# Performance work log

Measured on AMD Instinct MI355X. Metric: run time of the kernel, lower is better.

Reference implementation:

```python
import jax, jax.numpy as jnp
import numpy as np

SL, BS, E, H, PF, STRIDE, SHIFT = 2048, 2, 1024, 16, 16, 1, 0
DH = E // H  # 64


def setup_inputs() -> dict:
    key = jax.random.key(0)
    ks = jax.random.split(key, 6)
    s = 0.02
    return {
        'x': jax.random.normal(ks[0], (SL, BS, E), jnp.float32),
        'ln_g': jnp.ones((E,), jnp.float32),
        'ln_b': jnp.zeros((E,), jnp.float32),
        'Wq': jax.random.normal(ks[1], (E, E), jnp.float32) * s,
        'bq': jnp.zeros((E,), jnp.float32),
        'Wk': jax.random.normal(ks[2], (E, E), jnp.float32) * s,
        'bk': jnp.zeros((E,), jnp.float32),
        'Wv': jax.random.normal(ks[3], (E, E), jnp.float32) * s,
        'bv': jnp.zeros((E,), jnp.float32),
        'Wo': jax.random.normal(ks[4], (E, E), jnp.float32) * s,
        'bo': jnp.zeros((E,), jnp.float32),
    }


def _layernorm(x, g, b, eps=1e-5):
    m = x.mean(-1, keepdims=True)
    v = jnp.var(x, axis=-1, keepdims=True)
    return (x - m) * jax.lax.rsqrt(v + eps) * g + b


def _sparsify(context, h):
    # faithful to sparsify(): r = (arange(h)+1)*stride - pf + shift (+ arange(pf)), mod c
    c = context.shape[0]
    base = (jnp.arange(h) + 1) * STRIDE - PF + SHIFT          # [h]
    idx = (base[None, :] + jnp.arange(PF)[:, None]) % c       # [pf, h]
    return context[idx.reshape(-1)].reshape(PF, h, context.shape[1], context.shape[2])


def reference(x, ln_g, ln_b, Wq, bq, Wk, bk, Wv, bv, Wo, bo):
    sl, bs, e = x.shape
    residual = x
    xn = _layernorm(x, ln_g, ln_b)
    # gather pf-sized local context window per query position (modular wrap)
    fetch = _sparsify(xn, sl)                                  # [pf, sl, bs, E]
    # per-token query (length-1) attending to its pf gathered keys
    q = (xn @ Wq + bq).reshape(sl, bs, H, DH)                  # [sl,bs,H,dh]
    k = (fetch @ Wk + bk).reshape(PF, sl, bs, H, DH)           # [pf,sl,bs,H,dh]
    v = (fetch @ Wv + bv).reshape(PF, sl, bs, H, DH)
    scale = 1.0 / jnp.sqrt(jnp.float32(DH))
    scores = jnp.einsum('sbhd,psbhd->sbhp', q, k) * scale      # [sl,bs,H,pf]
    attn = jax.nn.softmax(scores, axis=-1)
    out = jnp.einsum('sbhp,psbhd->sbhd', attn, v).reshape(sl, bs, e)
    out = out @ Wo + bo                                        # output projection
    # dropout is a no-op in eval
    return residual + out
```

## Files before the change

### kernel.cpp

```cpp
#include <hip/hip_runtime.h>
#include <cstdint>
#include <cstddef>

#define SLEN 2048
#define BSZ  2
#define EDIM 1024
#define NHEAD 16
#define DHEAD 64
#define PFW  16
#define NTOK (SLEN*BSZ)

typedef __attribute__((ext_vector_type(8))) short short8;
typedef __attribute__((ext_vector_type(4))) float floatx4;
typedef __attribute__((ext_vector_type(4))) int   int4v;

__device__ __forceinline__ short f2bf(float f) {
  union { float f; uint32_t u; } v; v.f = f;
  uint32_t r = v.u + 0x7fffu + ((v.u >> 16) & 1u);
  return (short)(r >> 16);
}
__device__ __forceinline__ float bf2f(short s) {
  union { uint32_t u; float f; } v; v.u = ((uint32_t)(uint16_t)s) << 16;
  return v.f;
}
__device__ __forceinline__ int q8(float f, float inv) {
  int q = __float2int_rn(f * inv);
  return min(127, max(-127, q));
}

__device__ __forceinline__ void async16(const void* g, void* l) {
  __builtin_amdgcn_global_load_lds((const __attribute__((address_space(1))) void*)g,
                                   (__attribute__((address_space(3))) void*)l,
                                   16, 0, 0);
}

#define VMCNT(n) asm volatile("s_waitcnt vmcnt(" #n ")" ::: "memory")

__global__ __launch_bounds__(256) void prep_kernel(
    const float* __restrict__ x, const float* __restrict__ g,
    const float* __restrict__ b, char* __restrict__ xn_i8,
    float* __restrict__ xn_scl,
    const float* __restrict__ W0, const float* __restrict__ W1,
    const float* __restrict__ W2, const float* __restrict__ W3,
    short* __restrict__ Wt_base)
{
  const int bid = blockIdx.x;
  const int tid = threadIdx.x;

  if (bid < NTOK) {
    const int row = bid;
    const float4 v = ((const float4*)(x + (size_t)row * EDIM))[tid];
    float s  = v.x + v.y + v.z + v.w;
    float ss = v.x * v.x + v.y * v.y + v.z * v.z + v.w * v.w;
#pragma unroll
    for (int off = 32; off; off >>= 1) {
      s  += __shfl_xor(s, off);
      ss += __shfl_xor(ss, off);
    }
    __shared__ float ws_s[4], ws_ss[4], ws_m[4];
    const int lane = tid & 63, wave = tid >> 6;
    if (lane == 0) { ws_s[wave] = s; ws_ss[wave] = ss; }
    __syncthreads();
    s  = ws_s[0] + ws_s[1] + ws_s[2] + ws_s[3];
    ss = ws_ss[0] + ws_ss[1] + ws_ss[2] + ws_ss[3];

    const float mean = s * (1.0f / EDIM);
    const float var  = ss * (1.0f / EDIM) - mean * mean;
    const float rs   = rsqrtf(var + 1e-5f);

    const float4 gv = ((const float4*)g)[tid];
    const float4 bv = ((const float4*)b)[tid];
    const float n0 = (v.x - mean) * rs * gv.x + bv.x;
    const float n1 = (v.y - mean) * rs * gv.y + bv.y;
    const float n2 = (v.z - mean) * rs * gv.z + bv.z;
    const float n3 = (v.w - mean) * rs * gv.w + bv.w;

    float am = fmaxf(fmaxf(fabsf(n0), fabsf(n1)), fmaxf(fabsf(n2), fabsf(n3)));
#pragma unroll
    for (int off = 32; off; off >>= 1) am = fmaxf(am, __shfl_xor(am, off));
    if (lane == 0) ws_m[wave] = am;
    __syncthreads();
    am = fmaxf(fmaxf(ws_m[0], ws_m[1]), fmaxf(ws_m[2], ws_m[3]));

    const float inv = (am > 1e-30f) ? 127.0f / am : 0.0f;
    const int q0 = q8(n0, inv), q1 = q8(n1, inv), q2 = q8(n2, inv), q3 = q8(n3, inv);
    const uint32_t pack = (uint32_t)(q0 & 0xff) | ((uint32_t)(q1 & 0xff) << 8) |
                          ((uint32_t)(q2 & 0xff) << 16) | ((uint32_t)(q3 & 0xff) << 24);
    ((uint32_t*)(xn_i8 + (size_t)row * EDIM))[tid] = pack;
    if (tid == 0) xn_scl[row] = am * (1.0f / 127.0f);
  } else {
    const int t = bid - NTOK;
    const int z = t >> 10;
    const int rem = t & 1023;
    const int n0 = (rem & 31) * 32;
    const int k0 = (rem >> 5) * 32;
    const float* W = (z == 0) ? W0 : (z == 1) ? W1 : (z == 2) ? W2 : W3;
    short* Wt = Wt_base + (size_t)z * EDIM * EDIM;

    __shared__ float tile[32][33];
    const int tx = tid & 31;
    const int ty = tid >> 5;
#pragma unroll
    for (int i = 0; i < 4; ++i)
      tile[ty + i * 8][tx] = W[(size_t)(k0 + ty + i * 8) * EDIM + n0 + tx];
    __syncthreads();
#pragma unroll
    for (int i = 0; i < 4; ++i)
      Wt[(size_t)(n0 + ty + i * 8) * EDIM + k0 + tx] = f2bf(tile[tx][ty + i * 8]);
  }
}

__global__ __launch_bounds__(256) void quant_w(
    const short* __restrict__ Wt, char* __restrict__ w_i8,
    float* __restrict__ w_scl)
{
  const int R = blockIdx.x;
  const int tid = threadIdx.x;
  const short4 s4 = ((const short4*)(Wt + (size_t)R * EDIM))[tid];
  const float w0 = bf2f(s4.x), w1 = bf2f(s4.y), w2 = bf2f(s4.z), w3 = bf2f(s4.w);

  float am = fmaxf(fmaxf(fabsf(w0), fabsf(w1)), fmaxf(fabsf(w2), fabsf(w3)));
#pragma unroll
  for (int off = 32; off; off >>= 1) am = fmaxf(am, __shfl_xor(am, off));
  __shared__ float wm[4];
  const int lane = tid & 63, wave = tid >> 6;
  if (lane == 0) wm[wave] = am;
  __syncthreads();
  am = fmaxf(fmaxf(wm[0], wm[1]), fmaxf(wm[2], wm[3]));

  const float inv = (am > 1e-30f) ? 127.0f / am : 0.0f;
  const int q0 = q8(w0, inv), q1 = q8(w1, inv), q2 = q8(w2, inv), q3 = q8(w3, inv);
  const uint32_t pack = (uint32_t)(q0 & 0xff) | ((uint32_t)(q1 & 0xff) << 8) |
                        ((uint32_t)(q2 & 0xff) << 16) | ((uint32_t)(q3 & 0xff) << 24);
  ((uint32_t*)(w_i8 + (size_t)R * EDIM))[tid] = pack;
  if (tid == 0) w_scl[R] = am * (1.0f / 127.0f);
}

__global__ __launch_bounds__(512, 2) void gemm_qkv256(
    const char* __restrict__ xn_i8, const float* __restrict__ xn_scl,
    const char* __restrict__ w_i8, const float* __restrict__ w_scl,
    const float* __restrict__ bq, const float* __restrict__ bk,
    const float* __restrict__ bv, short* __restrict__ qkv_base)
{
  __shared__ __align__(16) char lds[4][32768];

  const int bid = blockIdx.x;
  const int lin = (bid & 7) * 24 + (bid >> 3);
  const int mt  = lin & 15;
  const int nt  = lin >> 4;
  const int z   = nt >> 2;
  const int bm  = mt * 256;
  const int bnz = (nt & 3) * 256;

  const float* bias = (z == 0) ? bq : (z == 1) ? bk : bv;
  short* out = qkv_base + (size_t)z * NTOK * EDIM;

  const int tid = threadIdx.x;
  const int wv  = tid >> 6;
  const int ln  = tid & 63;
  const int q   = ln >> 4;
  const int l16 = ln & 15;
  const int wm  = wv >> 2;
  const int wn  = wv & 3;

  const int sr = tid >> 2;
  const int sc = ((tid & 3) * 16) ^ ((sr & 3) * 16);
  const char* gA0 = xn_i8 + (size_t)(bm + sr) * EDIM + sc;
  const char* gA1 = gA0 + (size_t)128 * EDIM;
  const char* gB0 = w_i8 + ((size_t)z << 20) + (size_t)(bnz + sr) * EDIM + sc;
  const char* gB1 = gB0 + (size_t)128 * EDIM;
  const int wbase = wv * 1024;

#define QSTAGE(tt) do { \
    char* s_ = lds[(tt) & 3]; \
    async16(gA0 + (tt) * 64, s_ + wbase); \
    async16(gA1 + (tt) * 64, s_ + 8192 + wbase); \
    async16(gB0 + (tt) * 64, s_ + 16384 + wbase); \
    async16(gB1 + (tt) * 64, s_ + 24576 + wbase); \
  } while (0)

  const int swz  = (q * 16) ^ ((l16 & 3) * 16);
  const int aoff = (wm * 128 + l16) * 64 + swz;
  const int boff = 16384 + (wn * 64 + l16) * 64 + swz;

  int4v acc[8][4];
#pragma unroll
  for (int mi = 0; mi < 8; ++mi)
#pragma unroll
    for (int ni = 0; ni < 4; ++ni) { int4v zz = {0, 0, 0, 0}; acc[mi][ni] = zz; }

  QSTAGE(0); QSTAGE(1); QSTAGE(2);
  VMCNT(8);
  __builtin_amdgcn_s_barrier();
  __builtin_amdgcn_sched_barrier(0);

#pragma unroll
  for (int t = 0; t < 16; ++t) {
    if (t + 3 < 16) QSTAGE(t + 3);

    const char* sl = lds[t & 3];
    int4v bf[4], af[8];
#pragma unroll
    for (int ni = 0; ni < 4; ++ni)
      bf[ni] = *(const int4v*)(sl + boff + ni * 1024);
#pragma unroll
    for (int mi = 0; mi < 8; ++mi)
      af[mi] = *(const int4v*)(sl + aoff + mi * 1024);

    __builtin_amdgcn_s_setprio(1);
#pragma unroll
    for (int mi = 0; mi < 8; ++mi)
#pragma unroll
      for (int ni = 0; ni < 4; ++ni)
        acc[mi][ni] = __builtin_amdgcn_mfma_i32_16x16x64_i8(
            af[mi], bf[ni], acc[mi][ni], 0, 0, 0);
    __builtin_amdgcn_s_setprio(0);

    if (t < 15) {
      if (t <= 12)      VMCNT(8);
      else if (t == 13) VMCNT(4);
      else              VMCNT(0);
      __builtin_amdgcn_s_barrier();
      __builtin_amdgcn_sched_barrier(0);
    }
  }
#undef QSTAGE

  const int rbase = bm + wm * 128 + q * 4;
  const int cbl   = bnz + wn * 64 + l16;
#pragma unroll
  for (int mi = 0; mi < 8; ++mi) {
    float sa[4];
#pragma unroll
    for (int r = 0; r < 4; ++r) sa[r] = xn_scl[rbase + mi * 16 + r];
#pragma unroll
    for (int ni = 0; ni < 4; ++ni) {
      const int c  = cbl + ni * 16;
      const float sb = w_scl[z * EDIM + c];
      const float bb = bias[c];
      const int4v v = acc[mi][ni];
#pragma unroll
      for (int r = 0; r < 4; ++r)
        out[(size_t)(rbase + mi * 16 + r) * EDIM + c] =
            f2bf((float)v[r] * (sa[r] * sb) + bb);
    }
  }
}

__global__ __launch_bounds__(256) void gemm_o_bf16(
    const short* __restrict__ Abf, const short* __restrict__ Bt,
    const float* __restrict__ bo, const float* __restrict__ residual,
    float* __restrict__ out)
{
  __shared__ __align__(16) char ring[4][12288];

  const int bm = blockIdx.x * 64;
  const int bn = blockIdx.y * 128;
  const int tid  = threadIdx.x;
  const int lane = tid & 63;
  const int wave = tid >> 6;

  const int lrow = lane >> 2;
  const int scol = ((lane & 3) * 16) ^ ((lrow & 3) * 16);
  const char* gA0 = (const char*)Abf + (size_t)(bm + wave * 16 + lrow) * (EDIM * 2) + scol;
  const char* gB0 = (const char*)Bt  + (size_t)(bn + wave * 32 + lrow) * (EDIM * 2) + scol;
  const char* gB1 = gB0 + (size_t)16 * (EDIM * 2);
  const int aw = wave * 1024;
  const int bw = 4096 + wave * 2048;

#define OSTAGE(tt) do { \
    char* s_ = ring[(tt) & 3]; \
    async16(gA0 + (tt) * 64, s_ + aw); \
    async16(gB0 + (tt) * 64, s_ + bw); \
    async16(gB1 + (tt) * 64, s_ + bw + 1024); \
  } while (0)

  const int wm  = (wave >> 1) * 32;
  const int wn  = (wave & 1) * 64;
  const int l16 = lane & 15;
  const int q4  = lane >> 4;
  const int swz  = (q4 * 16) ^ ((l16 & 3) * 16);
  const int aoff = (wm + l16) * 64 + swz;
  const int boff = 4096 + (wn + l16) * 64 + swz;

  floatx4 facc[2][4];
#pragma unroll
  for (int i = 0; i < 2; ++i)
#pragma unroll
    for (int j = 0; j < 4; ++j) { floatx4 zz = {0.f, 0.f, 0.f, 0.f}; facc[i][j] = zz; }

  OSTAGE(0); OSTAGE(1); OSTAGE(2);
  VMCNT(6);
  __builtin_amdgcn_s_barrier();
  __builtin_amdgcn_sched_barrier(0);

#pragma unroll
  for (int t = 0; t < 32; ++t) {
    if (t + 3 < 32) OSTAGE(t + 3);

    const char* sl = ring[t & 3];
    short8 af[2], bf[4];
#pragma unroll
    for (int mi = 0; mi < 2; ++mi)
      af[mi] = *(const short8*)(sl + aoff + mi * 1024);
#pragma unroll
    for (int ni = 0; ni < 4; ++ni)
      bf[ni] = *(const short8*)(sl + boff + ni * 1024);

    __builtin_amdgcn_s_setprio(1);
#pragma unroll
    for (int mi = 0; mi < 2; ++mi)
#pragma unroll
      for (int ni = 0; ni < 4; ++ni)
        facc[mi][ni] = __builtin_amdgcn_mfma_f32_16x16x32_bf16(
            af[mi], bf[ni], facc[mi][ni], 0, 0, 0);
    __builtin_amdgcn_s_setprio(0);

    if (t < 31) {
      if (t <= 28)      VMCNT(6);
      else if (t == 29) VMCNT(3);
      else              VMCNT(0);
      __builtin_amdgcn_s_barrier();
      __builtin_amdgcn_sched_barrier(0);
    }
  }
#undef OSTAGE

  const int r0 = bm + wm + q4 * 4;
  const int c0 = bn + wn + l16;
#pragma unroll
  for (int mi = 0; mi < 2; ++mi)
#pragma unroll
    for (int ni = 0; ni < 4; ++ni) {
      const int col = c0 + ni * 16;
      const float bb = bo[col];
#pragma unroll
      for (int r = 0; r < 4; ++r) {
        const int row = r0 + mi * 16 + r;
        const size_t idx = (size_t)row * EDIM + col;
        out[idx] = residual[idx] + facc[mi][ni][r] + bb;
      }
    }
}

#define VT_LD 80
#define PB_LD 40

__global__ __launch_bounds__(256) void attn_mfma(
    const short* __restrict__ Q, const short* __restrict__ K,
    const short* __restrict__ V, short* __restrict__ Obf)
{
  const int tid  = threadIdx.x;
  const int lane = tid & 63;
  const int wave = tid >> 6;
  const int quad = lane >> 4;
  const int l16  = lane & 15;

  const int bh = blockIdx.y;
  const int h  = bh & (NHEAD - 1);
  const int b  = bh >> 4;
  const int s_blk = blockIdx.x * 64;
  const int col0  = h * DHEAD;

  __shared__ __align__(16) short VT[64 * VT_LD];
  __shared__ __align__(16) short Pb[4][16 * PB_LD];

  for (int task = tid; task < 320; task += 256) {
    const int kp  = task >> 3;
    const int dg  = task & 7;
    const int kk0 = kp * 2;
    int sA = s_blk - 15 + kk0;
    int sB = sA + 1;
    if (sA < 0) sA += SLEN;  if (sA >= SLEN) sA -= SLEN;
    if (sB < 0) sB += SLEN;  if (sB >= SLEN) sB -= SLEN;
    const short8 vA = *(const short8*)(V + (size_t)(sA * BSZ + b) * EDIM + col0 + dg * 8);
    const short8 vB = *(const short8*)(V + (size_t)(sB * BSZ + b) * EDIM + col0 + dg * 8);
#pragma unroll
    for (int j = 0; j < 8; ++j) {
      const int d = dg * 8 + j;
      const uint32_t pack = (uint32_t)(uint16_t)vA[j] | ((uint32_t)(uint16_t)vB[j] << 16);
      *(uint32_t*)&VT[d * VT_LD + kk0] = pack;
    }
  }

  const int sw = s_blk + wave * 16;
  short8 aq[2];
  {
    const size_t base = (size_t)((sw + l16) * BSZ + b) * EDIM + col0 + quad * 8;
    aq[0] = *(const short8*)(Q + base);
    aq[1] = *(const short8*)(Q + base + 32);
  }
  short8 bkf[2][2];
#pragma unroll
  for (int T = 0; T < 2; ++T) {
    int ks = sw - 15 + T * 16 + l16;
    if (ks < 0) ks += SLEN;
    if (ks >= SLEN) ks -= SLEN;
    const size_t base = (size_t)(ks * BSZ + b) * EDIM + col0 + quad * 8;
    bkf[T][0] = *(const short8*)(K + base);
    bkf[T][1] = *(const short8*)(K + base + 32);
  }

  floatx4 S[2];
  { floatx4 zz = {0.f, 0.f, 0.f, 0.f}; S[0] = zz; S[1] = zz; }
#pragma unroll
  for (int T = 0; T < 2; ++T) {
    S[T] = __builtin_amdgcn_mfma_f32_16x16x32_bf16(aq[0], bkf[T][0], S[T], 0, 0, 0);
    S[T] = __builtin_amdgcn_mfma_f32_16x16x32_bf16(aq[1], bkf[T][1], S[T], 0, 0, 0);
  }

  float sc[2][4];
#pragma unroll
  for (int T = 0; T < 2; ++T)
#pragma unroll
    for (int r = 0; r < 4; ++r) {
      const int m = quad * 4 + r;
      const int c = T * 16 + l16;
      const int d = c - m;
      sc[T][r] = (d >= 0 && d <= 15) ? S[T][r] * 0.125f : -1e30f;
    }
  float mx[4], sm[4];
#pragma unroll
  for (int r = 0; r < 4; ++r) mx[r] = fmaxf(sc[0][r], sc[1][r]);
#pragma unroll
  for (int off = 1; off <= 8; off <<= 1)
#pragma unroll
    for (int r = 0; r < 4; ++r) mx[r] = fmaxf(mx[r], __shfl_xor(mx[r], off));
  float p[2][4];
#pragma unroll
  for (int r = 0; r < 4; ++r) {
    p[0][r] = __expf(sc[0][r] - mx[r]);
    p[1][r] = __expf(sc[1][r] - mx[r]);
    sm[r] = p[0][r] + p[1][r];
  }
#pragma unroll
  for (int off = 1; off <= 8; off <<= 1)
#pragma unroll
    for (int r = 0; r < 4; ++r) sm[r] += __shfl_xor(sm[r], off);

  __syncthreads();

  short* Pw = Pb[wave];
#pragma unroll
  for (int T = 0; T < 2; ++T)
#pragma unroll
    for (int r = 0; r < 4; ++r) {
      const int m = quad * 4 + r;
      const int c = T * 16 + l16;
      Pw[m * PB_LD + c] = f2bf(p[T][r]);
    }
  __syncthreads();
  const short8 ap = *(const short8*)(Pw + l16 * PB_LD + quad * 8);

  floatx4 Oacc[4];
  { floatx4 zz = {0.f, 0.f, 0.f, 0.f}; Oacc[0] = zz; Oacc[1] = zz; Oacc[2] = zz; Oacc[3] = zz; }
#pragma unroll
  for (int nt = 0; nt < 4; ++nt) {
    const short8 bv = *(const short8*)(VT + (nt * 16 + l16) * VT_LD + wave * 16 + quad * 8);
    Oacc[nt] = __builtin_amdgcn_mfma_f32_16x16x32_bf16(ap, bv, Oacc[nt], 0, 0, 0);
  }

  float ism[4];
#pragma unroll
  for (int r = 0; r < 4; ++r) ism[r] = 1.0f / sm[r];
#pragma unroll
  for (int nt = 0; nt < 4; ++nt)
#pragma unroll
    for (int r = 0; r < 4; ++r) {
      const int m = quad * 4 + r;
      const int row = (sw + m) * BSZ + b;
      Obf[(size_t)row * EDIM + col0 + nt * 16 + l16] = f2bf(Oacc[nt][r] * ism[r]);
    }
}

extern "C" void kernel_launch(void* const* d_in, const int* in_sizes, int n_in,
                              void* d_out, int out_size, void* d_ws, size_t ws_size,
                              hipStream_t stream) {
  const float* x    = (const float*)d_in[0];
  const float* ln_g = (const float*)d_in[1];
  const float* ln_b = (const float*)d_in[2];
  const float* Wq   = (const float*)d_in[3];
  const float* bq   = (const float*)d_in[4];
  const float* Wk   = (const float*)d_in[5];
  const float* bk   = (const float*)d_in[6];
  const float* Wv   = (const float*)d_in[7];
  const float* bv   = (const float*)d_in[8];
  const float* Wo   = (const float*)d_in[9];
  const float* bo   = (const float*)d_in[10];
  float* out = (float*)d_out;

  char* ws = (char*)d_ws;
  char*  xn_i8   = ws;
  short* Wt      = (short*)(ws + ((size_t)4  << 20));
  char*  w_i8    = ws + ((size_t)12 << 20);
  short* QKV     = (short*)(ws + ((size_t)16 << 20));
  float* xn_scl  = (float*)(ws + ((size_t)44 << 20));
  float* w_scl   = (float*)(ws + ((size_t)44 << 20) + (1 << 16));
  short* Obf     = (short*)ws;

  prep_kernel<<<NTOK + 4096, 256, 0, stream>>>(x, ln_g, ln_b, xn_i8, xn_scl,
                                               Wq, Wk, Wv, Wo, Wt);
  quant_w<<<3 * EDIM, 256, 0, stream>>>(Wt, w_i8, w_scl);
  gemm_qkv256<<<192, 512, 0, stream>>>(xn_i8, xn_scl, w_i8, w_scl,
                                       bq, bk, bv, QKV);
  attn_mfma<<<dim3(SLEN / 64, BSZ * NHEAD), 256, 0, stream>>>(
      QKV, QKV + (size_t)NTOK * EDIM, QKV + (size_t)2 * NTOK * EDIM, Obf);
  gemm_o_bf16<<<dim3(NTOK / 64, EDIM / 128), 256, 0, stream>>>(
      Obf, Wt + (size_t)3 * EDIM * EDIM, bo, x, out);
}
```

Before: 149.2 us.

## Fuse all stages into a persistent megakernel with grid-wide barriers

Replaces the five separate kernel launches (layernorm/quantize, weight transpose, weight quantize, QKV GEMM, attention, output GEMM) with one persistent 256-block kernel. The stages are separated by a software grid barrier built on atomic flags in the workspace, which is reset with a memset before each launch. The goal is to remove launch overhead and inter-kernel gaps. In exchange, stages now run with a fixed grid of 256 blocks at 512 threads, which may under-occupy some phases. It also relies on all blocks being co-resident, or the barrier can deadlock.

```diff
diff --git a/kernel.cpp b/kernel.cpp
--- a/kernel.cpp
+++ b/kernel.cpp
@@ -7,7 +7,6 @@
 #define EDIM 1024
 #define NHEAD 16
 #define DHEAD 64
-#define PFW  16
 #define NTOK (SLEN*BSZ)
 
 typedef __attribute__((ext_vector_type(8))) short short8;
@@ -27,450 +26,502 @@
   int q = __float2int_rn(f * inv);
   return min(127, max(-127, q));
 }
-
 __device__ __forceinline__ void async16(const void* g, void* l) {
   __builtin_amdgcn_global_load_lds((const __attribute__((address_space(1))) void*)g,
                                    (__attribute__((address_space(3))) void*)l,
                                    16, 0, 0);
 }
-
 #define VMCNT(n) asm volatile("s_waitcnt vmcnt(" #n ")" ::: "memory")
 
-__global__ __launch_bounds__(256) void prep_kernel(
-    const float* __restrict__ x, const float* __restrict__ g,
-    const float* __restrict__ b, char* __restrict__ xn_i8,
-    float* __restrict__ xn_scl,
-    const float* __restrict__ W0, const float* __restrict__ W1,
-    const float* __restrict__ W2, const float* __restrict__ W3,
-    short* __restrict__ Wt_base)
+__device__ __forceinline__ void grid_bar(uint32_t* flags, uint32_t* go,
+                                         int phase, int bid, int tid) {
+  __syncthreads();
+  if (bid == 0) {
+    if (tid > 0 && tid < 256) {
+      while (__hip_atomic_load(&flags[tid], __ATOMIC_ACQUIRE,
+                               __HIP_MEMORY_SCOPE_AGENT) < (uint32_t)phase)
+        __builtin_amdgcn_s_sleep(1);
+    }
+    __syncthreads();
+    if (tid == 0)
+      __hip_atomic_store(go, (uint32_t)phase, __ATOMIC_RELEASE,
+                         __HIP_MEMORY_SCOPE_AGENT);
+  } else {
+    if (tid == 0) {
+      __hip_atomic_store(&flags[bid], (uint32_t)phase, __ATOMIC_RELEASE,
+                         __HIP_MEMORY_SCOPE_AGENT);
+      while (__hip_atomic_load(go, __ATOMIC_ACQUIRE,
+                               __HIP_MEMORY_SCOPE_AGENT) < (uint32_t)phase)
+        __builtin_amdgcn_s_sleep(1);
+    }
+  }
+  __syncthreads();
+}
+
+#define VT_LD 80
+#define PB_LD 40
+
+__global__ __launch_bounds__(512, 2) void mega(
+    const float* __restrict__ x, const float* __restrict__ ln_g,
+    const float* __restrict__ ln_b,
+    const float* __restrict__ Wq, const float* __restrict__ bq,
+    const float* __restrict__ Wk, const float* __restrict__ bk,
+    const float* __restrict__ Wv, const float* __restrict__ bv,
+    const float* __restrict__ Wo, const float* __restrict__ bo,
+    char* xn_i8, float* xn_scl, short* Wt_base, char* w_i8, float* w_scl,
+    short* qkv_base, short* Obf, float* __restrict__ out,
+    uint32_t* bar)
 {
-  const int bid = blockIdx.x;
-  const int tid = threadIdx.x;
-
-  if (bid < NTOK) {
-    const int row = bid;
-    const float4 v = ((const float4*)(x + (size_t)row * EDIM))[tid];
-    float s  = v.x + v.y + v.z + v.w;
-    float ss = v.x * v.x + v.y * v.y + v.z * v.z + v.w * v.w;
-#pragma unroll
-    for (int off = 32; off; off >>= 1) {
-      s  += __shfl_xor(s, off);
-      ss += __shfl_xor(ss, off);
-    }
-    __shared__ float ws_s[4], ws_ss[4], ws_m[4];
-    const int lane = tid & 63, wave = tid >> 6;
-    if (lane == 0) { ws_s[wave] = s; ws_ss[wave] = ss; }
-    __syncthreads();
-    s  = ws_s[0] + ws_s[1] + ws_s[2] + ws_s[3];
-    ss = ws_ss[0] + ws_ss[1] + ws_ss[2] + ws_ss[3];
-
-    const float mean = s * (1.0f / EDIM);
-    const float var  = ss * (1.0f / EDIM) - mean * mean;
-    const float rs   = rsqrtf(var + 1e-5f);
-
-    const float4 gv = ((const float4*)g)[tid];
-    const float4 bv = ((const float4*)b)[tid];
-    const float n0 = (v.x - mean) * rs * gv.x + bv.x;
-    const float n1 = (v.y - mean) * rs * gv.y + bv.y;
-    const float n2 = (v.z - mean) * rs * gv.z + bv.z;
-    const float n3 = (v.w - mean) * rs * gv.w + bv.w;
-
-    float am = fmaxf(fmaxf(fabsf(n0), fabsf(n1)), fmaxf(fabsf(n2), fabsf(n3)));
-#pragma unroll
-    for (int off = 32; off; off >>= 1) am = fmaxf(am, __shfl_xor(am, off));
-    if (lane == 0) ws_m[wave] = am;
-    __syncthreads();
-    am = fmaxf(fmaxf(ws_m[0], ws_m[1]), fmaxf(ws_m[2], ws_m[3]));
-
-    const float inv = (am > 1e-30f) ? 127.0f / am : 0.0f;
-    const int q0 = q8(n0, inv), q1 = q8(n1, inv), q2 = q8(n2, inv), q3 = q8(n3, inv);
-    const uint32_t pack = (uint32_t)(q0 & 0xff) | ((uint32_t)(q1 & 0xff) << 8) |
-                          ((uint32_t)(q2 & 0xff) << 16) | ((uint32_t)(q3 & 0xff) << 24);
-    ((uint32_t*)(xn_i8 + (size_t)row * EDIM))[tid] = pack;
-    if (tid == 0) xn_scl[row] = am * (1.0f / 127.0f);
-  } else {
-    const int t = bid - NTOK;
-    const int z = t >> 10;
-    const int rem = t & 1023;
-    const int n0 = (rem & 31) * 32;
-    const int k0 = (rem >> 5) * 32;
-    const float* W = (z == 0) ? W0 : (z == 1) ? W1 : (z == 2) ? W2 : W3;
-    short* Wt = Wt_base + (size_t)z * EDIM * EDIM;
-
-    __shared__ float tile[32][33];
-    const int tx = tid & 31;
-    const int ty = tid >> 5;
-#pragma unroll
-    for (int i = 0; i < 4; ++i)
-      tile[ty + i * 8][tx] = W[(size_t)(k0 + ty + i * 8) * EDIM + n0 + tx];
-    __syncthreads();
-#pragma unroll
-    for (int i = 0; i < 4; ++i)
-      Wt[(size_t)(n0 + ty + i * 8) * EDIM + k0 + tx] = f2bf(tile[tx][ty + i * 8]);
-  }
-}
-
-__global__ __launch_bounds__(256) void quant_w(
-    const short* __restrict__ Wt, char* __restrict__ w_i8,
-    float* __restrict__ w_scl)
-{
-  const int R = blockIdx.x;
-  const int tid = threadIdx.x;
-  const short4 s4 = ((const short4*)(Wt + (size_t)R * EDIM))[tid];
-  const float w0 = bf2f(s4.x), w1 = bf2f(s4.y), w2 = bf2f(s4.z), w3 = bf2f(s4.w);
-
-  float am = fmaxf(fmaxf(fabsf(w0), fabsf(w1)), fmaxf(fabsf(w2), fabsf(w3)));
-#pragma unroll
-  for (int off = 32; off; off >>= 1) am = fmaxf(am, __shfl_xor(am, off));
-  __shared__ float wm[4];
-  const int lane = tid & 63, wave = tid >> 6;
-  if (lane == 0) wm[wave] = am;
-  __syncthreads();
-  am = fmaxf(fmaxf(wm[0], wm[1]), fmaxf(wm[2], wm[3]));
-
-  const float inv = (am > 1e-30f) ? 127.0f / am : 0.0f;
-  const int q0 = q8(w0, inv), q1 = q8(w1, inv), q2 = q8(w2, inv), q3 = q8(w3, inv);
-  const uint32_t pack = (uint32_t)(q0 & 0xff) | ((uint32_t)(q1 & 0xff) << 8) |
-                        ((uint32_t)(q2 & 0xff) << 16) | ((uint32_t)(q3 & 0xff) << 24);
-  ((uint32_t*)(w_i8 + (size_t)R * EDIM))[tid] = pack;
-  if (tid == 0) w_scl[R] = am * (1.0f / 127.0f);
-}
-
-__global__ __launch_bounds__(512, 2) void gemm_qkv256(
-    const char* __restrict__ xn_i8, const float* __restrict__ xn_scl,
-    const char* __restrict__ w_i8, const float* __restrict__ w_scl,
-    const float* __restrict__ bq, const float* __restrict__ bk,
-    const float* __restrict__ bv, short* __restrict__ qkv_base)
-{
-  __shared__ __align__(16) char lds[4][32768];
-
-  const int bid = blockIdx.x;
-  const int lin = (bid & 7) * 24 + (bid >> 3);
-  const int mt  = lin & 15;
-  const int nt  = lin >> 4;
-  const int z   = nt >> 2;
-  const int bm  = mt * 256;
-  const int bnz = (nt & 3) * 256;
-
-  const float* bias = (z == 0) ? bq : (z == 1) ? bk : bv;
-  short* out = qkv_base + (size_t)z * NTOK * EDIM;
-
-  const int tid = threadIdx.x;
-  const int wv  = tid >> 6;
-  const int ln  = tid & 63;
-  const int q   = ln >> 4;
-  const int l16 = ln & 15;
-  const int wm  = wv >> 2;
-  const int wn  = wv & 3;
-
-  const int sr = tid >> 2;
-  const int sc = ((tid & 3) * 16) ^ ((sr & 3) * 16);
-  const char* gA0 = xn_i8 + (size_t)(bm + sr) * EDIM + sc;
-  const char* gA1 = gA0 + (size_t)128 * EDIM;
-  const char* gB0 = w_i8 + ((size_t)z << 20) + (size_t)(bnz + sr) * EDIM + sc;
-  const char* gB1 = gB0 + (size_t)128 * EDIM;
-  const int wbase = wv * 1024;
+  __shared__ __align__(16) char smem[131072];
+
+  const int tid  = threadIdx.x;
+  const int bid  = blockIdx.x;
+  const int wv   = tid >> 6;
+  const int ln   = tid & 63;
+  const int half = tid >> 8;
+  const int t256 = tid & 255;
+
+  uint32_t* flags = bar;
+  uint32_t* go    = bar + 256;
+
+  {
+    const int gw = bid * 8 + wv;
+#pragma unroll
+    for (int rr = 0; rr < 2; ++rr) {
+      const int row = gw + rr * 2048;
+      const float* xr = x + (size_t)row * EDIM;
+      float4 v[4];
+#pragma unroll
+      for (int c = 0; c < 4; ++c) v[c] = ((const float4*)xr)[c * 64 + ln];
+      float s = 0.f, ss = 0.f;
+#pragma unroll
+      for (int c = 0; c < 4; ++c) {
+        s  += v[c].x + v[c].y + v[c].z + v[c].w;
+        ss += v[c].x*v[c].x + v[c].y*v[c].y + v[c].z*v[c].z + v[c].w*v[c].w;
+      }
+#pragma unroll
+      for (int off = 32; off; off >>= 1) {
+        s += __shfl_xor(s, off); ss += __shfl_xor(ss, off);
+      }
+      const float mean = s * (1.0f / EDIM);
+      const float var  = ss * (1.0f / EDIM) - mean * mean;
+      const float rs   = rsqrtf(var + 1e-5f);
+
+      float n[16]; float am = 0.f;
+#pragma unroll
+      for (int c = 0; c < 4; ++c) {
+        const float4 gv = ((const float4*)ln_g)[c * 64 + ln];
+        const float4 bv = ((const float4*)ln_b)[c * 64 + ln];
+        n[c*4+0] = (v[c].x - mean) * rs * gv.x + bv.x;
+        n[c*4+1] = (v[c].y - mean) * rs * gv.y + bv.y;
+        n[c*4+2] = (v[c].z - mean) * rs * gv.z + bv.z;
+        n[c*4+3] = (v[c].w - mean) * rs * gv.w + bv.w;
+        am = fmaxf(am, fmaxf(fmaxf(fabsf(n[c*4+0]), fabsf(n[c*4+1])),
+                             fmaxf(fabsf(n[c*4+2]), fabsf(n[c*4+3]))));
+      }
+#pragma unroll
+      for (int off = 32; off; off >>= 1) am = fmaxf(am, __shfl_xor(am, off));
+      const float inv = (am > 1e-30f) ? 127.0f / am : 0.0f;
+#pragma unroll
+      for (int c = 0; c < 4; ++c) {
+        const uint32_t pk =
+            (uint32_t)(q8(n[c*4+0], inv) & 0xff)        |
+            ((uint32_t)(q8(n[c*4+1], inv) & 0xff) << 8) |
+            ((uint32_t)(q8(n[c*4+2], inv) & 0xff) << 16)|
+            ((uint32_t)(q8(n[c*4+3], inv) & 0xff) << 24);
+        ((uint32_t*)(xn_i8 + (size_t)row * EDIM))[c * 64 + ln] = pk;
+      }
+      if (ln == 0) xn_scl[row] = am * (1.0f / 127.0f);
+    }
+  }
+
+  {
+    float (*tile)[33] = (float (*)[33])(smem + half * 8448);
+    const int tx = t256 & 31;
+    const int ty = t256 >> 5;
+    for (int it = 0; it < 8; ++it) {
+      const int tl  = bid * 16 + it * 2 + half;
+      const int z   = tl >> 10;
+      const int rem = tl & 1023;
+      const int n0  = (rem & 31) * 32;
+      const int k0  = (rem >> 5) * 32;
+      const float* W = (z == 0) ? Wq : (z == 1) ? Wk : (z == 2) ? Wv : Wo;
+      short* Wt = Wt_base + (size_t)z * EDIM * EDIM;
+#pragma unroll
+      for (int i = 0; i < 4; ++i)
+        tile[ty + i * 8][tx] = W[(size_t)(k0 + ty + i * 8) * EDIM + n0 + tx];
+      __syncthreads();
+#pragma unroll
+      for (int i = 0; i < 4; ++i)
+        Wt[(size_t)(n0 + ty + i * 8) * EDIM + k0 + tx] = f2bf(tile[tx][ty + i * 8]);
+      __syncthreads();
+    }
+  }
+
+  grid_bar(flags, go, 1, bid, tid);
+
+  {
+    const int gw = bid * 8 + wv;
+#pragma unroll
+    for (int rr = 0; rr < 2; ++rr) {
+      const int row = gw + rr * 2048;
+      if (row < 3 * EDIM) {
+        const short* wr = Wt_base + (size_t)row * EDIM;
+        float w[16]; float am = 0.f;
+#pragma unroll
+        for (int c = 0; c < 4; ++c) {
+          const short4 sv = ((const short4*)wr)[c * 64 + ln];
+          w[c*4+0] = bf2f(sv.x); w[c*4+1] = bf2f(sv.y);
+          w[c*4+2] = bf2f(sv.z); w[c*4+3] = bf2f(sv.w);
+          am = fmaxf(am, fmaxf(fmaxf(fabsf(w[c*4+0]), fabsf(w[c*4+1])),
+                               fmaxf(fabsf(w[c*4+2]), fabsf(w[c*4+3]))));
+        }
+#pragma unroll
+        for (int off = 32; off; off >>= 1) am = fmaxf(am, __shfl_xor(am, off));
+        const float inv = (am > 1e-30f) ? 127.0f / am : 0.0f;
+#pragma unroll
+        for (int c = 0; c < 4; ++c) {
+          const uint32_t pk =
+              (uint32_t)(q8(w[c*4+0], inv) & 0xff)        |
+              ((uint32_t)(q8(w[c*4+1], inv) & 0xff) << 8) |
+              ((uint32_t)(q8(w[c*4+2], inv) & 0xff) << 16)|
+              ((uint32_t)(q8(w[c*4+3], inv) & 0xff) << 24);
+          ((uint32_t*)(w_i8 + (size_t)row * EDIM))[c * 64 + ln] = pk;
+        }
+        if (ln == 0) w_scl[row] = am * (1.0f / 127.0f);
+      }
+    }
+  }
+
+  grid_bar(flags, go, 2, bid, tid);
+
+  if (bid < 192) {
+    char* qlds = smem;
+    const int lin = (bid & 7) * 24 + (bid >> 3);
+    const int mt  = lin & 15;
+    const int nt  = lin >> 4;
+    const int z   = nt >> 2;
+    const int bm  = mt * 256;
+    const int bnz = (nt & 3) * 256;
+
+    const float* bias = (z == 0) ? bq : (z == 1) ? bk : bv;
+    short* o = qkv_base + (size_t)z * NTOK * EDIM;
+
+    const int q   = ln >> 4;
+    const int l16 = ln & 15;
+    const int wm  = wv >> 2;
+    const int wn  = wv & 3;
+
+    const int sr = tid >> 2;
+    const int sc = ((tid & 3) * 16) ^ ((sr & 3) * 16);
+    const char* gA0 = xn_i8 + (size_t)(bm + sr) * EDIM + sc;
+    const char* gA1 = gA0 + (size_t)128 * EDIM;
+    const char* gB0 = w_i8 + ((size_t)z << 20) + (size_t)(bnz + sr) * EDIM + sc;
+    const char* gB1 = gB0 + (size_t)128 * EDIM;
+    const int wbase = wv * 1024;
 
 #define QSTAGE(tt) do { \
-    char* s_ = lds[(tt) & 3]; \
+    char* s_ = qlds + ((tt) & 3) * 32768; \
     async16(gA0 + (tt) * 64, s_ + wbase); \
     async16(gA1 + (tt) * 64, s_ + 8192 + wbase); \
     async16(gB0 + (tt) * 64, s_ + 16384 + wbase); \
     async16(gB1 + (tt) * 64, s_ + 24576 + wbase); \
   } while (0)
 
-  const int swz  = (q * 16) ^ ((l16 & 3) * 16);
-  const int aoff = (wm * 128 + l16) * 64 + swz;
-  const int boff = 16384 + (wn * 64 + l16) * 64 + swz;
-
-  int4v acc[8][4];
-#pragma unroll
-  for (int mi = 0; mi < 8; ++mi)
-#pragma unroll
-    for (int ni = 0; ni < 4; ++ni) { int4v zz = {0, 0, 0, 0}; acc[mi][ni] = zz; }
-
-  QSTAGE(0); QSTAGE(1); QSTAGE(2);
-  VMCNT(8);
-  __builtin_amdgcn_s_barrier();
-  __builtin_amdgcn_sched_barrier(0);
-
-#pragma unroll
-  for (int t = 0; t < 16; ++t) {
-    if (t + 3 < 16) QSTAGE(t + 3);
-
-    const char* sl = lds[t & 3];
-    int4v bf[4], af[8];
-#pragma unroll
-    for (int ni = 0; ni < 4; ++ni)
-      bf[ni] = *(const int4v*)(sl + boff + ni * 1024);
+    const int swz  = (q * 16) ^ ((l16 & 3) * 16);
+    const int aoff = (wm * 128 + l16) * 64 + swz;
+    const int boff = 16384 + (wn * 64 + l16) * 64 + swz;
+
+    int4v acc[8][4];
 #pragma unroll
     for (int mi = 0; mi < 8; ++mi)
-      af[mi] = *(const int4v*)(sl + aoff + mi * 1024);
-
-    __builtin_amdgcn_s_setprio(1);
-#pragma unroll
-    for (int mi = 0; mi < 8; ++mi)
+#pragma unroll
+      for (int ni = 0; ni < 4; ++ni) { int4v zz = {0,0,0,0}; acc[mi][ni] = zz; }
+
+    QSTAGE(0); QSTAGE(1); QSTAGE(2);
+    VMCNT(8);
+    __builtin_amdgcn_s_barrier();
+    __builtin_amdgcn_sched_barrier(0);
+
+#pragma unroll
+    for (int t = 0; t < 16; ++t) {
+      if (t + 3 < 16) QSTAGE(t + 3);
+
+      const char* sl = qlds + (t & 3) * 32768;
+      int4v bf[4], af[8];
 #pragma unroll
       for (int ni = 0; ni < 4; ++ni)
-        acc[mi][ni] = __builtin_amdgcn_mfma_i32_16x16x64_i8(
-            af[mi], bf[ni], acc[mi][ni], 0, 0, 0);
-    __builtin_amdgcn_s_setprio(0);
-
-    if (t < 15) {
-      if (t <= 12)      VMCNT(8);
-      else if (t == 13) VMCNT(4);
-      else              VMCNT(0);
-      __builtin_amdgcn_s_barrier();
-      __builtin_amdgcn_sched_barrier(0);
-    }
-  }
+        bf[ni] = *(const int4v*)(sl + boff + ni * 1024);
+#pragma unroll
+      for (int mi = 0; mi < 8; ++mi)
+        af[mi] = *(const int4v*)(sl + aoff + mi * 1024);
+
+      __builtin_amdgcn_s_setprio(1);
+#pragma unroll
+      for (int mi = 0; mi < 8; ++mi)
+#pragma unroll
+        for (int ni = 0; ni < 4; ++ni)
+          acc[mi][ni] = __builtin_amdgcn_mfma_i32_16x16x64_i8(
+              af[mi], bf[ni], acc[mi][ni], 0, 0, 0);
+      __builtin_amdgcn_s_setprio(0);
+
+      if (t < 15) {
+        if (t <= 12)      VMCNT(8);
+        else if (t == 13) VMCNT(4);
+        else              VMCNT(0);
+        __builtin_amdgcn_s_barrier();
+        __builtin_amdgcn_sched_barrier(0);
+      }
+    }
 #undef QSTAGE
 
-  const int rbase = bm + wm * 128 + q * 4;
-  const int cbl   = bnz + wn * 64 + l16;
-#pragma unroll
-  for (int mi = 0; mi < 8; ++mi) {
-    float sa[4];
-#pragma unroll
-    for (int r = 0; r < 4; ++r) sa[r] = xn_scl[rbase + mi * 16 + r];
-#pragma unroll
-    for (int ni = 0; ni < 4; ++ni) {
-      const int c  = cbl + ni * 16;
-      const float sb = w_scl[z * EDIM + c];
-      const float bb = bias[c];
-      const int4v v = acc[mi][ni];
-#pragma unroll
-      for (int r = 0; r < 4; ++r)
-        out[(size_t)(rbase + mi * 16 + r) * EDIM + c] =
-            f2bf((float)v[r] * (sa[r] * sb) + bb);
-    }
-  }
-}
-
-__global__ __launch_bounds__(256) void gemm_o_bf16(
-    const short* __restrict__ Abf, const short* __restrict__ Bt,
-    const float* __restrict__ bo, const float* __restrict__ residual,
-    float* __restrict__ out)
-{
-  __shared__ __align__(16) char ring[4][12288];
-
-  const int bm = blockIdx.x * 64;
-  const int bn = blockIdx.y * 128;
-  const int tid  = threadIdx.x;
-  const int lane = tid & 63;
-  const int wave = tid >> 6;
-
-  const int lrow = lane >> 2;
-  const int scol = ((lane & 3) * 16) ^ ((lrow & 3) * 16);
-  const char* gA0 = (const char*)Abf + (size_t)(bm + wave * 16 + lrow) * (EDIM * 2) + scol;
-  const char* gB0 = (const char*)Bt  + (size_t)(bn + wave * 32 + lrow) * (EDIM * 2) + scol;
-  const char* gB1 = gB0 + (size_t)16 * (EDIM * 2);
-  const int aw = wave * 1024;
-  const int bw = 4096 + wave * 2048;
+    const int rbase = bm + wm * 128 + q * 4;
+    const int cbl   = bnz + wn * 64 + l16;
+#pragma unroll
+    for (int mi = 0; mi < 8; ++mi) {
+      float sa[4];
+#pragma unroll
+      for (int r = 0; r < 4; ++r) sa[r] = xn_scl[rbase + mi * 16 + r];
+#pragma unroll
+      for (int ni = 0; ni < 4; ++ni) {
+        const int c  = cbl + ni * 16;
+        const float sb = w_scl[z * EDIM + c];
+        const float bb = bias[c];
+        const int4v v = acc[mi][ni];
+#pragma unroll
+        for (int r = 0; r < 4; ++r)
+          o[(size_t)(rbase + mi * 16 + r) * EDIM + c] =
+              f2bf((float)v[r] * (sa[r] * sb) + bb);
+      }
+    }
+  }
+
+  grid_bar(flags, go, 3, bid, tid);
+
+  {
+    const short* Q = qkv_base;
+    const short* K = qkv_base + (size_t)NTOK * EDIM;
+    const short* V = qkv_base + (size_t)2 * NTOK * EDIM;
+    short* VT = (short*)(smem + half * 10240);
+    short* Pb = (short*)(smem + 20480 + half * 5120);
+
+    const int wave = t256 >> 6;
+    const int lane = tid & 63;
+    const int quad = lane >> 4;
+    const int l16  = lane & 15;
+
+    for (int it = 0; it < 2; ++it) {
+      const int unit  = bid * 4 + it * 2 + half;
+      const int bh    = unit >> 5;
+      const int h     = bh & (NHEAD - 1);
+      const int b     = bh >> 4;
+      const int s_blk = (unit & 31) * 64;
+      const int col0  = h * DHEAD;
+
+      __syncthreads();
+
+      for (int task = t256; task < 320; task += 256) {
+        const int kp  = task >> 3;
+        const int dg  = task & 7;
+        const int kk0 = kp * 2;
+        int sA = s_blk - 15 + kk0;
+        int sB = sA + 1;
+        if (sA < 0) sA += SLEN;  if (sA >= SLEN) sA -= SLEN;
+        if (sB < 0) sB += SLEN;  if (sB >= SLEN) sB -= SLEN;
+        const short8 vA = *(const short8*)(V + (size_t)(sA * BSZ + b) * EDIM + col0 + dg * 8);
+        const short8 vB = *(const short8*)(V + (size_t)(sB * BSZ + b) * EDIM + col0 + dg * 8);
+#pragma unroll
+        for (int j = 0; j < 8; ++j) {
+          const int d = dg * 8 + j;
+          const uint32_t pack = (uint32_t)(uint16_t)vA[j] | ((uint32_t)(uint16_t)vB[j] << 16);
+          *(uint32_t*)&VT[d * VT_LD + kk0] = pack;
+        }
+      }
+
+      const int sw = s_blk + wave * 16;
+      short8 aq[2];
+      {
+        const size_t base = (size_t)((sw + l16) * BSZ + b) * EDIM + col0 + quad * 8;
+        aq[0] = *(const short8*)(Q + base);
+        aq[1] = *(const short8*)(Q + base + 32);
+      }
+      short8 bkf[2][2];
+#pragma unroll
+      for (int T = 0; T < 2; ++T) {
+        int ks = sw - 15 + T * 16 + l16;
+        if (ks < 0) ks += SLEN;
+        if (ks >= SLEN) ks -= SLEN;
+        const size_t base = (size_t)(ks * BSZ + b) * EDIM + col0 + quad * 8;
+        bkf[T][0] = *(const short8*)(K + base);
+        bkf[T][1] = *(const short8*)(K + base + 32);
+      }
+
+      floatx4 S[2];
+      { floatx4 zz = {0.f,0.f,0.f,0.f}; S[0] = zz; S[1] = zz; }
+#pragma unroll
+      for (int T = 0; T < 2; ++T) {
+        S[T] = __builtin_amdgcn_mfma_f32_16x16x32_bf16(aq[0], bkf[T][0], S[T], 0, 0, 0);
+        S[T] = __builtin_amdgcn_mfma_f32_16x16x32_bf16(aq[1], bkf[T][1], S[T], 0, 0, 0);
+      }
+
+      float sc[2][4];
+#pragma unroll
+      for (int T = 0; T < 2; ++T)
+#pragma unroll
+        for (int r = 0; r < 4; ++r) {
+          const int m = quad * 4 + r;
+          const int c = T * 16 + l16;
+          const int d = c - m;
+          sc[T][r] = (d >= 0 && d <= 15) ? S[T][r] * 0.125f : -1e30f;
+        }
+      float mx[4], sm[4];
+#pragma unroll
+      for (int r = 0; r < 4; ++r) mx[r] = fmaxf(sc[0][r], sc[1][r]);
+#pragma unroll
+      for (int off = 1; off <= 8; off <<= 1)
+#pragma unroll
+        for (int r = 0; r < 4; ++r) mx[r] = fmaxf(mx[r], __shfl_xor(mx[r], off));
+      float p[2][4];
+#pragma unroll
+      for (int r = 0; r < 4; ++r) {
+        p[0][r] = __expf(sc[0][r] - mx[r]);
+        p[1][r] = __expf(sc[1][r] - mx[r]);
+        sm[r] = p[0][r] + p[1][r];
+      }
+#pragma unroll
+      for (int off = 1; off <= 8; off <<= 1)
+#pragma unroll
+        for (int r = 0; r < 4; ++r) sm[r] += __shfl_xor(sm[r], off);
+
+      __syncthreads();
+
+      short* Pw = Pb + wave * (16 * PB_LD);
+#pragma unroll
+      for (int T = 0; T < 2; ++T)
+#pragma unroll
+        for (int r = 0; r < 4; ++r) {
+          const int m = quad * 4 + r;
+          const int c = T * 16 + l16;
+          Pw[m * PB_LD + c] = f2bf(p[T][r]);
+        }
+      __syncthreads();
+      const short8 ap = *(const short8*)(Pw + l16 * PB_LD + quad * 8);
+
+      floatx4 Oacc[4];
+      { floatx4 zz = {0.f,0.f,0.f,0.f}; Oacc[0]=zz; Oacc[1]=zz; Oacc[2]=zz; Oacc[3]=zz; }
+#pragma unroll
+      for (int nt = 0; nt < 4; ++nt) {
+        const short8 bv = *(const short8*)(VT + (nt * 16 + l16) * VT_LD + wave * 16 + quad * 8);
+        Oacc[nt] = __builtin_amdgcn_mfma_f32_16x16x32_bf16(ap, bv, Oacc[nt], 0, 0, 0);
+      }
+
+      float ism[4];
+#pragma unroll
+      for (int r = 0; r < 4; ++r) ism[r] = 1.0f / sm[r];
+#pragma unroll
+      for (int nt = 0; nt < 4; ++nt)
+#pragma unroll
+        for (int r = 0; r < 4; ++r) {
+          const int m = quad * 4 + r;
+          const int row = (sw + m) * BSZ + b;
+          Obf[(size_t)row * EDIM + col0 + nt * 16 + l16] = f2bf(Oacc[nt][r] * ism[r]);
+        }
+    }
+  }
+
+  grid_bar(flags, go, 4, bid, tid);
+
+  {
+    const short* Bt = Wt_base + (size_t)3 * EDIM * EDIM;
+    char* ring = smem + half * 49152;
+    const int unit = bid * 2 + half;
+    const int bm = (unit & 63) * 64;
+    const int bn = (unit >> 6) * 128;
+    const int wave = t256 >> 6;
+    const int lane = tid & 63;
+
+    const int lrow = lane >> 2;
+    const int scol = ((lane & 3) * 16) ^ ((lrow & 3) * 16);
+    const char* gA0 = (const char*)Obf + (size_t)(bm + wave * 16 + lrow) * (EDIM * 2) + scol;
+    const char* gB0 = (const char*)Bt  + (size_t)(bn + wave * 32 + lrow) * (EDIM * 2) + scol;
+    const char* gB1 = gB0 + (size_t)16 * (EDIM * 2);
+    const int aw = wave * 1024;
+    const int bw = 4096 + wave * 2048;
 
 #define OSTAGE(tt) do { \
-    char* s_ = ring[(tt) & 3]; \
+    char* s_ = ring + ((tt) & 3) * 12288; \
     async16(gA0 + (tt) * 64, s_ + aw); \
     async16(gB0 + (tt) * 64, s_ + bw); \
     async16(gB1 + (tt) * 64, s_ + bw + 1024); \
   } while (0)
 
-  const int wm  = (wave >> 1) * 32;
-  const int wn  = (wave & 1) * 64;
-  const int l16 = lane & 15;
-  const int q4  = lane >> 4;
-  const int swz  = (q4 * 16) ^ ((l16 & 3) * 16);
-  const int aoff = (wm + l16) * 64 + swz;
-  const int boff = 4096 + (wn + l16) * 64 + swz;
-
-  floatx4 facc[2][4];
-#pragma unroll
-  for (int i = 0; i < 2; ++i)
-#pragma unroll
-    for (int j = 0; j < 4; ++j) { floatx4 zz = {0.f, 0.f, 0.f, 0.f}; facc[i][j] = zz; }
-
-  OSTAGE(0); OSTAGE(1); OSTAGE(2);
-  VMCNT(6);
-  __builtin_amdgcn_s_barrier();
-  __builtin_amdgcn_sched_barrier(0);
-
-#pragma unroll
-  for (int t = 0; t < 32; ++t) {
-    if (t + 3 < 32) OSTAGE(t + 3);
-
-    const char* sl = ring[t & 3];
-    short8 af[2], bf[4];
+    const int wm  = (wave >> 1) * 32;
+    const int wn  = (wave & 1) * 64;
+    const int l16 = lane & 15;
+    const int q4  = lane >> 4;
+    const int swz  = (q4 * 16) ^ ((l16 & 3) * 16);
+    const int aoff = (wm + l16) * 64 + swz;
+    const int boff = 4096 + (wn + l16) * 64 + swz;
+
+    floatx4 facc[2][4];
+#pragma unroll
+    for (int i = 0; i < 2; ++i)
+#pragma unroll
+      for (int j = 0; j < 4; ++j) { floatx4 zz = {0.f,0.f,0.f,0.f}; facc[i][j] = zz; }
+
+    OSTAGE(0); OSTAGE(1); OSTAGE(2);
+    VMCNT(6);
+    __builtin_amdgcn_s_barrier();
+    __builtin_amdgcn_sched_barrier(0);
+
+#pragma unroll
+    for (int t = 0; t < 32; ++t) {
+      if (t + 3 < 32) OSTAGE(t + 3);
+
+      const char* sl = ring + (t & 3) * 12288;
+      short8 af[2], bf[4];
+#pragma unroll
+      for (int mi = 0; mi < 2; ++mi)
+        af[mi] = *(const short8*)(sl + aoff + mi * 1024);
+#pragma unroll
+      for (int ni = 0; ni < 4; ++ni)
+        bf[ni] = *(const short8*)(sl + boff + ni * 1024);
+
+      __builtin_amdgcn_s_setprio(1);
+#pragma unroll
+      for (int mi = 0; mi < 2; ++mi)
+#pragma unroll
+        for (int ni = 0; ni < 4; ++ni)
+          facc[mi][ni] = __builtin_amdgcn_mfma_f32_16x16x32_bf16(
+              af[mi], bf[ni], facc[mi][ni], 0, 0, 0);
+      __builtin_amdgcn_s_setprio(0);
+
+      if (t < 31) {
+        if (t <= 28)      VMCNT(6);
+        else if (t == 29) VMCNT(3);
+        else              VMCNT(0);
+        __builtin_amdgcn_s_barrier();
+        __builtin_amdgcn_sched_barrier(0);
+      }
+    }
+#undef OSTAGE
+
+    const int r0 = bm + wm + q4 * 4;
+    const int c0 = bn + wn + l16;
 #pragma unroll
     for (int mi = 0; mi < 2; ++mi)
-      af[mi] = *(const short8*)(sl + aoff + mi * 1024);
-#pragma unroll
-    for (int ni = 0; ni < 4; ++ni)
-      bf[ni] = *(const short8*)(sl + boff + ni * 1024);
-
-    __builtin_amdgcn_s_setprio(1);
-#pragma unroll
-    for (int mi = 0; mi < 2; ++mi)
-#pragma unroll
-      for (int ni = 0; ni < 4; ++ni)
-        facc[mi][ni] = __builtin_amdgcn_mfma_f32_16x16x32_bf16(
-            af[mi], bf[ni], facc[mi][ni], 0, 0, 0);
-    __builtin_amdgcn_s_setprio(0);
-
-    if (t < 31) {
-      if (t <= 28)      VMCNT(6);
-      else if (t == 29) VMCNT(3);
-      else              VMCNT(0);
-      __builtin_amdgcn_s_barrier();
-      __builtin_amdgcn_sched_barrier(0);
-    }
-  }
-#undef OSTAGE
-
-  const int r0 = bm + wm + q4 * 4;
-  const int c0 = bn + wn + l16;
-#pragma unroll
-  for (int mi = 0; mi < 2; ++mi)
-#pragma unroll
-    for (int ni = 0; ni < 4; ++ni) {
-      const int col = c0 + ni * 16;
-      const float bb = bo[col];
-#pragma unroll
-      for (int r = 0; r < 4; ++r) {
-        const int row = r0 + mi * 16 + r;
-        const size_t idx = (size_t)row * EDIM + col;
-        out[idx] = residual[idx] + facc[mi][ni][r] + bb;
-      }
-    }
-}
-
-#define VT_LD 80
-#define PB_LD 40
-
-__global__ __launch_bounds__(256) void attn_mfma(
-    const short* __restrict__ Q, const short* __restrict__ K,
-    const short* __restrict__ V, short* __restrict__ Obf)
-{
-  const int tid  = threadIdx.x;
-  const int lane = tid & 63;
-  const int wave = tid >> 6;
-  const int quad = lane >> 4;
-  const int l16  = lane & 15;
-
-  const int bh = blockIdx.y;
-  const int h  = bh & (NHEAD - 1);
-  const int b  = bh >> 4;
-  const int s_blk = blockIdx.x * 64;
-  const int col0  = h * DHEAD;
-
-  __shared__ __align__(16) short VT[64 * VT_LD];
-  __shared__ __align__(16) short Pb[4][16 * PB_LD];
-
-  for (int task = tid; task < 320; task += 256) {
-    const int kp  = task >> 3;
-    const int dg  = task & 7;
-    const int kk0 = kp * 2;
-    int sA = s_blk - 15 + kk0;
-    int sB = sA + 1;
-    if (sA < 0) sA += SLEN;  if (sA >= SLEN) sA -= SLEN;
-    if (sB < 0) sB += SLEN;  if (sB >= SLEN) sB -= SLEN;
-    const short8 vA = *(const short8*)(V + (size_t)(sA * BSZ + b) * EDIM + col0 + dg * 8);
-    const short8 vB = *(const short8*)(V + (size_t)(sB * BSZ + b) * EDIM + col0 + dg * 8);
-#pragma unroll
-    for (int j = 0; j < 8; ++j) {
-      const int d = dg * 8 + j;
-      const uint32_t pack = (uint32_t)(uint16_t)vA[j] | ((uint32_t)(uint16_t)vB[j] << 16);
-      *(uint32_t*)&VT[d * VT_LD + kk0] = pack;
-    }
-  }
-
-  const int sw = s_blk + wave * 16;
-  short8 aq[2];
-  {
-    const size_t base = (size_t)((sw + l16) * BSZ + b) * EDIM + col0 + quad * 8;
-    aq[0] = *(const short8*)(Q + base);
-    aq[1] = *(const short8*)(Q + base + 32);
-  }
-  short8 bkf[2][2];
-#pragma unroll
-  for (int T = 0; T < 2; ++T) {
-    int ks = sw - 15 + T * 16 + l16;
-    if (ks < 0) ks += SLEN;
-    if (ks >= SLEN) ks -= SLEN;
-    const size_t base = (size_t)(ks * BSZ + b) * EDIM + col0 + quad * 8;
-    bkf[T][0] = *(const short8*)(K + base);
-    bkf[T][1] = *(const short8*)(K + base + 32);
-  }
-
-  floatx4 S[2];
-  { floatx4 zz = {0.f, 0.f, 0.f, 0.f}; S[0] = zz; S[1] = zz; }
-#pragma unroll
-  for (int T = 0; T < 2; ++T) {
-    S[T] = __builtin_amdgcn_mfma_f32_16x16x32_bf16(aq[0], bkf[T][0], S[T], 0, 0, 0);
-    S[T] = __builtin_amdgcn_mfma_f32_16x16x32_bf16(aq[1], bkf[T][1], S[T], 0, 0, 0);
-  }
-
-  float sc[2][4];
-#pragma unroll
-  for (int T = 0; T < 2; ++T)
-#pragma unroll
-    for (int r = 0; r < 4; ++r) {
-      const int m = quad * 4 + r;
-      const int c = T * 16 + l16;
-      const int d = c - m;
-      sc[T][r] = (d >= 0 && d <= 15) ? S[T][r] * 0.125f : -1e30f;
-    }
-  float mx[4], sm[4];
-#pragma unroll
-  for (int r = 0; r < 4; ++r) mx[r] = fmaxf(sc[0][r], sc[1][r]);
-#pragma unroll
-  for (int off = 1; off <= 8; off <<= 1)
-#pragma unroll
-    for (int r = 0; r < 4; ++r) mx[r] = fmaxf(mx[r], __shfl_xor(mx[r], off));
-  float p[2][4];
-#pragma unroll
-  for (int r = 0; r < 4; ++r) {
-    p[0][r] = __expf(sc[0][r] - mx[r]);
-    p[1][r] = __expf(sc[1][r] - mx[r]);
-    sm[r] = p[0][r] + p[1][r];
-  }
-#pragma unroll
-  for (int off = 1; off <= 8; off <<= 1)
-#pragma unroll
-    for (int r = 0; r < 4; ++r) sm[r] += __shfl_xor(sm[r], off);
-
-  __syncthreads();
-
-  short* Pw = Pb[wave];
-#pragma unroll
-  for (int T = 0; T < 2; ++T)
-#pragma unroll
-    for (int r = 0; r < 4; ++r) {
-      const int m = quad * 4 + r;
-      const int c = T * 16 + l16;
-      Pw[m * PB_LD + c] = f2bf(p[T][r]);
-    }
-  __syncthreads();
-  const short8 ap = *(const short8*)(Pw + l16 * PB_LD + quad * 8);
-
-  floatx4 Oacc[4];
-  { floatx4 zz = {0.f, 0.f, 0.f, 0.f}; Oacc[0] = zz; Oacc[1] = zz; Oacc[2] = zz; Oacc[3] = zz; }
-#pragma unroll
-  for (int nt = 0; nt < 4; ++nt) {
-    const short8 bv = *(const short8*)(VT + (nt * 16 + l16) * VT_LD + wave * 16 + quad * 8);
-    Oacc[nt] = __builtin_amdgcn_mfma_f32_16x16x32_bf16(ap, bv, Oacc[nt], 0, 0, 0);
-  }
-
-  float ism[4];
-#pragma unroll
-  for (int r = 0; r < 4; ++r) ism[r] = 1.0f / sm[r];
-#pragma unroll
-  for (int nt = 0; nt < 4; ++nt)
-#pragma unroll
-    for (int r = 0; r < 4; ++r) {
-      const int m = quad * 4 + r;
-      const int row = (sw + m) * BSZ + b;
-      Obf[(size_t)row * EDIM + col0 + nt * 16 + l16] = f2bf(Oacc[nt][r] * ism[r]);
-    }
+#pragma unroll
+      for (int ni = 0; ni < 4; ++ni) {
+        const int col = c0 + ni * 16;
+        const float bb = bo[col];
+#pragma unroll
+        for (int r = 0; r < 4; ++r) {
+          const int row = r0 + mi * 16 + r;
+          const size_t idx = (size_t)row * EDIM + col;
+          out[idx] = x[idx] + facc[mi][ni][r] + bb;
+        }
+      }
+  }
 }
 
 extern "C" void kernel_launch(void* const* d_in, const int* in_sizes, int n_in,
@@ -496,15 +547,11 @@
   short* QKV     = (short*)(ws + ((size_t)16 << 20));
   float* xn_scl  = (float*)(ws + ((size_t)44 << 20));
   float* w_scl   = (float*)(ws + ((size_t)44 << 20) + (1 << 16));
+  uint32_t* bar  = (uint32_t*)(ws + ((size_t)45 << 20));
   short* Obf     = (short*)ws;
 
-  prep_kernel<<<NTOK + 4096, 256, 0, stream>>>(x, ln_g, ln_b, xn_i8, xn_scl,
-                                               Wq, Wk, Wv, Wo, Wt);
-  quant_w<<<3 * EDIM, 256, 0, stream>>>(Wt, w_i8, w_scl);
-  gemm_qkv256<<<192, 512, 0, stream>>>(xn_i8, xn_scl, w_i8, w_scl,
-                                       bq, bk, bv, QKV);
-  attn_mfma<<<dim3(SLEN / 64, BSZ * NHEAD), 256, 0, stream>>>(
-      QKV, QKV + (size_t)NTOK * EDIM, QKV + (size_t)2 * NTOK * EDIM, Obf);
-  gemm_o_bf16<<<dim3(NTOK / 64, EDIM / 128), 256, 0, stream>>>(
-      Obf, Wt + (size_t)3 * EDIM * EDIM, bo, x, out);
-}
+  hipMemsetAsync(bar, 0, 4096, stream);
+  mega<<<256, 512, 0, stream>>>(x, ln_g, ln_b, Wq, bq, Wk, bk, Wv, bv, Wo, bo,
+                                xn_i8, xn_scl, Wt, w_i8, w_scl,
+                                QKV, Obf, out, bar);
+}
```

Measured after the change: 305.1 us. 104% more time.
